# Performance work log

Measured on AMD Instinct MI355X. Metric: run time of the kernel, lower is better.

## Reference

```python
import jax, jax.numpy as jnp
import numpy as np

W_BITS = 8
A_BITS = 8


def sym_quant(x, num_bits):
    # Symmetric per-last-dim abs-max quantization (SymQuantizer.forward, ndim<=3,
    # layerwise=False): s = (2^(b-1)-1)/(max|x| + 1e-6); q = round(x*s)/(s+1e-6)
    max_abs = jnp.max(jnp.abs(x), axis=-1, keepdims=True)
    s = (2.0 ** (num_bits - 1) - 1.0) / (max_abs + 1e-6)
    return jnp.round(x * s) / (s + 1e-6)


def setup_inputs() -> dict:
    key = jax.random.key(0)
    kx, kw = jax.random.split(key)
    B, S, NX, NF = 4, 2048, 1600, 6400
    x = jax.random.normal(kx, (B, S, NX), dtype=jnp.float32)
    weight = 0.02 * jax.random.normal(kw, (NX, NF), dtype=jnp.float32)  # Conv1D: [nx, nf]
    bias = jnp.zeros((NF,), dtype=jnp.float32)
    return {"x": x, "weight": weight, "bias": bias}


def reference(x, weight, bias):
    # quantize weights per-row (over nf), quantize activations per-token (over nx)
    wq = sym_quant(weight, W_BITS)
    xq = sym_quant(x, A_BITS)
    # addmm(bias, x.view(-1, nx), weight) then reshape back
    return jnp.einsum("bsx,xf->bsf", xq, wq) + bias
```

## Files before the change

kernel.cpp:

```cpp
#include <hip/hip_runtime.h>
#include <stdint.h>

typedef _Float16 f16;
typedef _Float16 f16x4 __attribute__((ext_vector_type(4)));
typedef _Float16 f16x8 __attribute__((ext_vector_type(8)));
typedef float f32x4 __attribute__((ext_vector_type(4)));

#define K_DIM 1600
#define NF_DIM 6400
#define KPAD 1664
#define NKT 26
#define KPB (KPAD * 2)

#define BUFSZ 57344
#define BOFF 16384

__device__ __forceinline__ void async_copy16(const void* g, void* l) {
    __builtin_amdgcn_global_load_lds(
        (const __attribute__((address_space(1))) void*)(uintptr_t)g,
        (__attribute__((address_space(3))) void*)(uint32_t)(uintptr_t)l,
        16, 0, 0);
}

__device__ __forceinline__ float blockMax(float v, float* sm) {
#pragma unroll
    for (int off = 32; off > 0; off >>= 1)
        v = fmaxf(v, __shfl_down(v, off, 64));
    int wid = threadIdx.x >> 6, lane = threadIdx.x & 63;
    if (lane == 0) sm[wid] = v;
    __syncthreads();
    if (threadIdx.x == 0) {
        float m = sm[0];
        for (int i = 1; i < (int)(blockDim.x >> 6); ++i) m = fmaxf(m, sm[i]);
        sm[0] = m;
    }
    __syncthreads();
    return sm[0];
}

__global__ void quant_x_kernel(const float* __restrict__ x, f16* __restrict__ qx,
                               float* __restrict__ ax) {
    __shared__ float sm[4];
    size_t row = blockIdx.x;
    const float* xr = x + row * (size_t)K_DIM;
    float m = 0.f;
    const int n4 = K_DIM >> 2;
    for (int i = threadIdx.x; i < n4; i += blockDim.x) {
        float4 v = ((const float4*)xr)[i];
        m = fmaxf(fmaxf(fmaxf(fabsf(v.x), fabsf(v.y)), fmaxf(fabsf(v.z), fabsf(v.w))), m);
    }
    m = blockMax(m, sm);
    float s = 127.0f / (m + 1e-6f);
    if (threadIdx.x == 0) ax[row] = 1.0f / (s + 1e-6f);
    f16* qr = qx + row * (size_t)KPAD;
    for (int i = threadIdx.x; i < n4; i += blockDim.x) {
        float4 v = ((const float4*)xr)[i];
        f16x4 q;
        q[0] = (f16)rintf(v.x * s);
        q[1] = (f16)rintf(v.y * s);
        q[2] = (f16)rintf(v.z * s);
        q[3] = (f16)rintf(v.w * s);
        *(f16x4*)&qr[i * 4] = q;
    }
    if (threadIdx.x < 16) {
        f16x4 z = {};
        *(f16x4*)&qr[K_DIM + threadIdx.x * 4] = z;
    }
}

__global__ void wscale_kernel(const float* __restrict__ w, float* __restrict__ sw) {
    __shared__ float sm[4];
    size_t k = blockIdx.x;
    const float* wr = w + k * (size_t)NF_DIM;
    float m = 0.f;
    const int n4 = NF_DIM >> 2;
    for (int i = threadIdx.x; i < n4; i += blockDim.x) {
        float4 v = ((const float4*)wr)[i];
        m = fmaxf(fmaxf(fmaxf(fabsf(v.x), fabsf(v.y)), fmaxf(fabsf(v.z), fabsf(v.w))), m);
    }
    m = blockMax(m, sm);
    if (threadIdx.x == 0) sw[k] = 127.0f / (m + 1e-6f);
}

__global__ void wtq_kernel(const float* __restrict__ w, const float* __restrict__ sw,
                           f16* __restrict__ wqt) {
    __shared__ f16 t[64][80];
    int k0 = blockIdx.x * 64;
    int f0 = blockIdx.y * 64;
    int tid = threadIdx.x;
    if (k0 >= K_DIM) {
        int fr = tid >> 2;
        int ch = (tid & 3) << 4;
        float4 z = {};
        float4* dst = (float4*)&wqt[(size_t)(f0 + fr) * KPAD + k0 + ch];
        dst[0] = z;
        dst[1] = z;
        return;
    }
    int rr = tid >> 4;
    int cc = (tid & 15) << 2;
#pragma unroll
    for (int i = 0; i < 4; ++i) {
        int r = rr + i * 16;
        float s = sw[k0 + r];
        float inv = 1.0f / (s + 1e-6f);
        float4 v = *(const float4*)&w[(size_t)(k0 + r) * NF_DIM + f0 + cc];
        t[cc + 0][r] = (f16)(rintf(v.x * s) * inv);
        t[cc + 1][r] = (f16)(rintf(v.y * s) * inv);
        t[cc + 2][r] = (f16)(rintf(v.z * s) * inv);
        t[cc + 3][r] = (f16)(rintf(v.w * s) * inv);
    }
    __syncthreads();
    int fr = tid >> 2;
    int ch = (tid & 3) << 4;
    const float4* src = (const float4*)&t[fr][ch];
    float4* dst = (float4*)&wqt[(size_t)(f0 + fr) * KPAD + k0 + ch];
    dst[0] = src[0];
    dst[1] = src[1];
}

__global__ __launch_bounds__(512, 1) void gemm128x320(
    const f16* __restrict__ A,
    const f16* __restrict__ Bt,
    const float* __restrict__ ax,
    const float* __restrict__ bias,
    float* __restrict__ C, int M, int N) {
    extern __shared__ char lds[];

    const int tid = threadIdx.x;
    const int lane = tid & 63;
    const int wv = tid >> 6;
    const int wm = wv >> 2;
    const int wn = wv & 3;
    const int lr = lane & 15;
    const int lg = lane >> 4;

    const int bid = blockIdx.x;
    const int cpx = gridDim.x >> 3;
    const int swz = (bid & 7) * cpx + (bid >> 3);
    const int tm = swz & 63;
    const int tn = swz >> 6;
    const size_t m0 = (size_t)tm * 128, n0 = (size_t)tn * 320;

    const int srow8 = lane >> 3;
    const int sslot = (lane & 7) ^ srow8;
    const char* pA = (const char*)A + (m0 + (size_t)(wv * 8 + srow8)) * KPB + sslot * 16;
    const char* pB = (const char*)Bt + (n0 + (size_t)(wv * 8 + srow8)) * KPB + sslot * 16;
    const int L0 = wv * 1024 + lane * 16;

#define ST_A(bufo, t)                                                          \
    {                                                                          \
        const char* g_ = pA + (size_t)(t) * 128;                               \
        async_copy16(g_, lds + (bufo) + L0);                                   \
        async_copy16(g_ + (size_t)64 * KPB, lds + (bufo) + 8192 + L0);         \
    }
#define ST_B(bufo, t)                                                          \
    {                                                                          \
        const char* g_ = pB + (size_t)(t) * 128;                               \
        _Pragma("unroll") for (int c_ = 0; c_ < 5; ++c_)                       \
            async_copy16(g_ + (size_t)(c_ * 64) * KPB,                         \
                         lds + (bufo) + BOFF + c_ * 8192 + L0);                \
    }

    const int swz0 = ((lg) ^ (lr & 7)) << 4;
    const int swz1 = ((4 + lg) ^ (lr & 7)) << 4;
    const int rbA = (wm * 64 + lr) * 128;
    const int rbB = BOFF + wn * 10240 + lr * 128;

#define RD_A(dst, bufo, rowoff, sz)                                    \
    {                                                                  \
        const char* p_ = lds + (bufo) + rbA + (rowoff) + (sz);         \
        dst[0] = *(const f16x8*)(p_);                                  \
        dst[1] = *(const f16x8*)(p_ + 2048);                           \
    }
#define RD_B(dst, bufo, sz)                                            \
    {                                                                  \
        const char* p_ = lds + (bufo) + rbB + (sz);                    \
        _Pragma("unroll") for (int n_ = 0; n_ < 5; ++n_)               \
            dst[n_] = *(const f16x8*)(p_ + n_ * 2048);                 \
    }

#define BARRIER __builtin_amdgcn_s_barrier()
#define LGKM(n) asm volatile("s_waitcnt lgkmcnt(" #n ")" ::: "memory")
#define VM0 asm volatile("s_waitcnt vmcnt(0)" ::: "memory")
#define SB0 __builtin_amdgcn_sched_barrier(0)

#define MF25(AF, BF, R0)                                                          \
    {                                                                             \
        __builtin_amdgcn_s_setprio(1);                                            \
        _Pragma("unroll") for (int a_ = 0; a_ < 2; ++a_)                          \
        _Pragma("unroll") for (int n_ = 0; n_ < 5; ++n_)                          \
            acc[(R0) + a_][n_] = __builtin_amdgcn_mfma_f32_16x16x32_f16(          \
                AF[a_], BF[n_], acc[(R0) + a_][n_], 0, 0, 0);                     \
        __builtin_amdgcn_s_setprio(0);                                            \
    }

#define TILE(CUR, NXT, tcur, tnext)                                   \
    {                                                                 \
                     \
        RD_A(aN, CUR, 0, swz1);                                       \
        RD_B(B1, CUR, swz1);                                          \
        ST_A(NXT, tnext);                                             \
        LGKM(7); SB0;                               \
        MF25(aP, B0, 0);                                              \
                             \
        RD_A(aP, CUR, 4096, swz0);                                    \
        ST_B(NXT, tnext);                                             \
        LGKM(2); SB0;                               \
        MF25(aN, B1, 0);                                              \
                                           \
        RD_A(aN, CUR, 4096, swz1);                                    \
        LGKM(2); SB0;                         \
        MF25(aP, B0, 2);                                              \
            \
        VM0;                                                          \
        BARRIER; SB0;                           \
        RD_A(aP, NXT, 0, swz0);                                       \
        RD_B(B0, NXT, swz0);                                          \
        LGKM(7); SB0;                         \
        MF25(aN, B1, 2);                                              \
        BARRIER;                       \
    }

    f32x4 acc[4][5] = {};
    f16x8 aP[2], aN[2], B0[5], B1[5];

    ST_A(0, 0);
    ST_B(0, 0);
    VM0;
    BARRIER;
    RD_A(aP, 0, 0, swz0);
    RD_B(B0, 0, swz0);

    for (int i = 0; i < NKT / 2; ++i) {
        const int te = 2 * i + 1;
        const int to = (2 * i + 2 < NKT) ? 2 * i + 2 : NKT - 1;
        TILE(0, BUFSZ, 2 * i, te);
        TILE(BUFSZ, 0, 2 * i + 1, to);
    }
    asm volatile("s_waitcnt vmcnt(0) lgkmcnt(0)" ::: "memory");

    float bv[5];
#pragma unroll
    for (int n_ = 0; n_ < 5; ++n_) bv[n_] = bias[n0 + wn * 80 + n_ * 16 + lr];
#pragma unroll
    for (int a = 0; a < 4; ++a) {
#pragma unroll
        for (int j = 0; j < 4; ++j) {
            size_t row = m0 + wm * 64 + a * 16 + lg * 4 + j;
            float axv = ax[row];
            float* crow = C + row * (size_t)N + n0 + wn * 80;
#pragma unroll
            for (int n_ = 0; n_ < 5; ++n_)
                crow[n_ * 16 + lr] = acc[a][n_][j] * axv + bv[n_];
        }
    }
}

extern "C" void kernel_launch(void* const* d_in, const int* in_sizes, int n_in,
                              void* d_out, int out_size, void* d_ws, size_t ws_size,
                              hipStream_t stream) {
    const float* x = (const float*)d_in[0];
    const float* w = (const float*)d_in[1];
    const float* bias = (const float*)d_in[2];
    float* out = (float*)d_out;

    const int M = in_sizes[0] / K_DIM;
    const int N = NF_DIM;

    char* ws = (char*)d_ws;
    f16* qx = (f16*)ws;
    f16* wqt = (f16*)(ws + (size_t)M * KPAD * 2);
    float* ax = (float*)(ws + (size_t)M * KPAD * 2 + (size_t)N * KPAD * 2);
    float* sw = ax + M;

    quant_x_kernel<<<M, 256, 0, stream>>>(x, qx, ax);
    wscale_kernel<<<K_DIM, 256, 0, stream>>>(w, sw);
    wtq_kernel<<<dim3(KPAD / 64, NF_DIM / 64), 256, 0, stream>>>(w, sw, wqt);

    (void)hipFuncSetAttribute((const void*)gemm128x320,
                              hipFuncAttributeMaxDynamicSharedMemorySize, 2 * BUFSZ);
    gemm128x320<<<(M / 128) * (N / 320), 512, 2 * BUFSZ, stream>>>(qx, wqt, ax, bias, out, M, N);
}
```

Measured before the change: 254.9 us.

## Pre-swizzle quantized activations into MFMA fragment layout and load A directly to registers

The activation quantizer now processes 16 rows per block through LDS and writes the quantized values in a layout that already matches the per-lane MFMA A-fragment order. The GEMM then loads A fragments straight from global memory into registers, prefetching one K-tile ahead, and no longer stages A in LDS. Only B goes through a smaller double-buffered LDS. This removes the LDS traffic and bank pressure for A and restructures the wait and barrier schedule. In exchange it uses more VGPRs for the prefetched A fragments, relies on global-load latency being hidden, and the quantizer gains a large LDS footprint.

```diff
diff --git a/kernel.cpp b/kernel.cpp
--- a/kernel.cpp
+++ b/kernel.cpp
@@ -10,10 +10,10 @@
 #define NF_DIM 6400
 #define KPAD 1664
 #define NKT 26
+#define KB52 52
 #define KPB (KPAD * 2)
 
-#define BUFSZ 57344
-#define BOFF 16384
+#define BUFB 40960
 
 __device__ __forceinline__ void async_copy16(const void* g, void* l) {
     __builtin_amdgcn_global_load_lds(
@@ -38,33 +38,52 @@
     return sm[0];
 }
 
-__global__ void quant_x_kernel(const float* __restrict__ x, f16* __restrict__ qx,
+#define QSTRIDE 1604
+__global__ void quant_x_kernel(const float* __restrict__ x, f16* __restrict__ qxt,
                                float* __restrict__ ax) {
-    __shared__ float sm[4];
-    size_t row = blockIdx.x;
-    const float* xr = x + row * (size_t)K_DIM;
-    float m = 0.f;
-    const int n4 = K_DIM >> 2;
-    for (int i = threadIdx.x; i < n4; i += blockDim.x) {
-        float4 v = ((const float4*)xr)[i];
-        m = fmaxf(fmaxf(fmaxf(fabsf(v.x), fabsf(v.y)), fmaxf(fabsf(v.z), fabsf(v.w))), m);
-    }
-    m = blockMax(m, sm);
-    float s = 127.0f / (m + 1e-6f);
-    if (threadIdx.x == 0) ax[row] = 1.0f / (s + 1e-6f);
-    f16* qr = qx + row * (size_t)KPAD;
-    for (int i = threadIdx.x; i < n4; i += blockDim.x) {
-        float4 v = ((const float4*)xr)[i];
-        f16x4 q;
-        q[0] = (f16)rintf(v.x * s);
-        q[1] = (f16)rintf(v.y * s);
-        q[2] = (f16)rintf(v.z * s);
-        q[3] = (f16)rintf(v.w * s);
-        *(f16x4*)&qr[i * 4] = q;
-    }
-    if (threadIdx.x < 16) {
-        f16x4 z = {};
-        *(f16x4*)&qr[K_DIM + threadIdx.x * 4] = z;
+    extern __shared__ float xs[];
+    __shared__ float sm[16];
+    const int mb = blockIdx.x;
+    const int tid = threadIdx.x;
+    const float4* xb4 = (const float4*)(x + (size_t)mb * 16 * K_DIM);
+    float4* xs4 = (float4*)xs;
+#pragma unroll
+    for (int rr = 0; rr < 16; ++rr)
+        for (int i = tid; i < 400; i += 256)
+            xs4[rr * 401 + i] = xb4[rr * 400 + i];
+    __syncthreads();
+    {
+        int r = tid >> 4, si = tid & 15;
+        float m = 0.f;
+        const float4* row4 = (const float4*)(xs + r * QSTRIDE);
+        for (int j = si; j < 400; j += 16) {
+            float4 v = row4[j];
+            m = fmaxf(fmaxf(fmaxf(fabsf(v.x), fabsf(v.y)), fmaxf(fabsf(v.z), fabsf(v.w))), m);
+        }
+#pragma unroll
+        for (int o = 8; o > 0; o >>= 1) m = fmaxf(m, __shfl_xor(m, o, 64));
+        if (si == 0) sm[r] = m;
+    }
+    __syncthreads();
+    if (tid < 16) {
+        float s = 127.0f / (sm[tid] + 1e-6f);
+        ax[mb * 16 + tid] = 1.0f / (s + 1e-6f);
+        sm[tid] = s;
+    }
+    __syncthreads();
+    f16* outb = qxt + (size_t)mb * KB52 * 512;
+    for (int c = tid; c < KB52 * 64; c += 256) {
+        int kb = c >> 6, lane = c & 63;
+        int lr = lane & 15, lg = lane >> 4;
+        int k0 = kb * 32 + lg * 8;
+        f16x8 q = {};
+        if (k0 < K_DIM) {
+            float s = sm[lr];
+            const float* src = xs + lr * QSTRIDE + k0;
+#pragma unroll
+            for (int j = 0; j < 8; ++j) q[j] = (f16)rintf(src[j] * s);
+        }
+        *(f16x8*)(outb + (size_t)c * 8) = q;
     }
 }
 
@@ -119,8 +138,8 @@
     dst[1] = src[1];
 }
 
-__global__ __launch_bounds__(512, 1) void gemm128x320(
-    const f16* __restrict__ A,
+__global__ __launch_bounds__(512, 1) void gemm_ad(
+    const f16* __restrict__ Aq,
     const f16* __restrict__ Bt,
     const float* __restrict__ ax,
     const float* __restrict__ bias,
@@ -144,99 +163,88 @@
 
     const int srow8 = lane >> 3;
     const int sslot = (lane & 7) ^ srow8;
-    const char* pA = (const char*)A + (m0 + (size_t)(wv * 8 + srow8)) * KPB + sslot * 16;
     const char* pB = (const char*)Bt + (n0 + (size_t)(wv * 8 + srow8)) * KPB + sslot * 16;
     const int L0 = wv * 1024 + lane * 16;
-
-#define ST_A(bufo, t)                                                          \
-    {                                                                          \
-        const char* g_ = pA + (size_t)(t) * 128;                               \
-        async_copy16(g_, lds + (bufo) + L0);                                   \
-        async_copy16(g_ + (size_t)64 * KPB, lds + (bufo) + 8192 + L0);         \
-    }
 #define ST_B(bufo, t)                                                          \
     {                                                                          \
         const char* g_ = pB + (size_t)(t) * 128;                               \
         _Pragma("unroll") for (int c_ = 0; c_ < 5; ++c_)                       \
             async_copy16(g_ + (size_t)(c_ * 64) * KPB,                         \
-                         lds + (bufo) + BOFF + c_ * 8192 + L0);                \
-    }
-
-    const int swz0 = ((lg) ^ (lr & 7)) << 4;
-    const int swz1 = ((4 + lg) ^ (lr & 7)) << 4;
-    const int rbA = (wm * 64 + lr) * 128;
-    const int rbB = BOFF + wn * 10240 + lr * 128;
-
-#define RD_A(dst, bufo, rowoff, sz)                                    \
-    {                                                                  \
-        const char* p_ = lds + (bufo) + rbA + (rowoff) + (sz);         \
-        dst[0] = *(const f16x8*)(p_);                                  \
-        dst[1] = *(const f16x8*)(p_ + 2048);                           \
-    }
-#define RD_B(dst, bufo, sz)                                            \
-    {                                                                  \
-        const char* p_ = lds + (bufo) + rbB + (sz);                    \
-        _Pragma("unroll") for (int n_ = 0; n_ < 5; ++n_)               \
-            dst[n_] = *(const f16x8*)(p_ + n_ * 2048);                 \
+                         lds + (bufo) + c_ * 8192 + L0);                       \
+    }
+
+    const f16* aBase = Aq + (size_t)(tm * 8 + wm * 4) * (KB52 * 512) + lane * 8;
+#define LD_A(dst, t)                                                           \
+    {                                                                          \
+        _Pragma("unroll") for (int p_ = 0; p_ < 4; ++p_)                       \
+        _Pragma("unroll") for (int kk_ = 0; kk_ < 2; ++kk_)                    \
+            dst[p_][kk_] = *(const f16x8*)(aBase +                             \
+                (size_t)(p_ * KB52 + 2 * (t) + kk_) * 512);                    \
+    }
+
+    const int bdr0 = (wn * 80 + lr) * 128 + (((lg) ^ (lr & 7)) << 4);
+    const int bdr1 = (wn * 80 + lr) * 128 + (((4 + lg) ^ (lr & 7)) << 4);
+#define RD_B5(dst, bufo, off)                                                  \
+    {                                                                          \
+        const char* p_ = lds + (bufo) + (off);                                 \
+        _Pragma("unroll") for (int n_ = 0; n_ < 5; ++n_)                       \
+            dst[n_] = *(const f16x8*)(p_ + n_ * 2048);                         \
     }
 
 #define BARRIER __builtin_amdgcn_s_barrier()
 #define LGKM(n) asm volatile("s_waitcnt lgkmcnt(" #n ")" ::: "memory")
-#define VM0 asm volatile("s_waitcnt vmcnt(0)" ::: "memory")
+#define VM13 asm volatile("s_waitcnt vmcnt(13)" ::: "memory")
 #define SB0 __builtin_amdgcn_sched_barrier(0)
 
-#define MF25(AF, BF, R0)                                                          \
+#define MF10(A0_, A1_, BF, R0)                                                    \
     {                                                                             \
         __builtin_amdgcn_s_setprio(1);                                            \
-        _Pragma("unroll") for (int a_ = 0; a_ < 2; ++a_)                          \
-        _Pragma("unroll") for (int n_ = 0; n_ < 5; ++n_)                          \
-            acc[(R0) + a_][n_] = __builtin_amdgcn_mfma_f32_16x16x32_f16(          \
-                AF[a_], BF[n_], acc[(R0) + a_][n_], 0, 0, 0);                     \
+        _Pragma("unroll") for (int n_ = 0; n_ < 5; ++n_) {                        \
+            acc[(R0)][n_] = __builtin_amdgcn_mfma_f32_16x16x32_f16(               \
+                A0_, BF[n_], acc[(R0)][n_], 0, 0, 0);                             \
+            acc[(R0) + 1][n_] = __builtin_amdgcn_mfma_f32_16x16x32_f16(           \
+                A1_, BF[n_], acc[(R0) + 1][n_], 0, 0, 0);                         \
+        }                                                                         \
         __builtin_amdgcn_s_setprio(0);                                            \
     }
 
-#define TILE(CUR, NXT, tcur, tnext)                                   \
+#define TILE(CUR, NXT, AC, AN, t1, t2)                                \
     {                                                                 \
-                     \
-        RD_A(aN, CUR, 0, swz1);                                       \
-        RD_B(B1, CUR, swz1);                                          \
-        ST_A(NXT, tnext);                                             \
-        LGKM(7); SB0;                               \
-        MF25(aP, B0, 0);                                              \
-                             \
-        RD_A(aP, CUR, 4096, swz0);                                    \
-        ST_B(NXT, tnext);                                             \
-        LGKM(2); SB0;                               \
-        MF25(aN, B1, 0);                                              \
-                                           \
-        RD_A(aN, CUR, 4096, swz1);                                    \
-        LGKM(2); SB0;                         \
-        MF25(aP, B0, 2);                                              \
-            \
-        VM0;                                                          \
-        BARRIER; SB0;                           \
-        RD_A(aP, NXT, 0, swz0);                                       \
-        RD_B(B0, NXT, swz0);                                          \
-        LGKM(7); SB0;                         \
-        MF25(aN, B1, 2);                                              \
-        BARRIER;                       \
+                                        \
+        LD_A(AN, t1);                                                 \
+        RD_B5(B1, CUR, bdr1);                                         \
+        LGKM(5); SB0;                                                 \
+        MF10(AC[0][0], AC[1][0], B0, 0);                              \
+                      \
+        LGKM(0); SB0;                                                 \
+        BARRIER;                                                      \
+        ST_B(CUR, t2); SB0;                                           \
+        MF10(AC[2][0], AC[3][0], B0, 2);                              \
+                                                   \
+        MF10(AC[0][1], AC[1][1], B1, 0);                              \
+               \
+        VM13; SB0;                                                    \
+        BARRIER;                                                      \
+        RD_B5(B0, NXT, bdr0); SB0;                                    \
+        MF10(AC[2][1], AC[3][1], B1, 2);                              \
     }
 
     f32x4 acc[4][5] = {};
-    f16x8 aP[2], aN[2], B0[5], B1[5];
-
-    ST_A(0, 0);
+    f16x8 aC[4][2], aN[4][2], B0[5], B1[5];
+
     ST_B(0, 0);
-    VM0;
+    ST_B(BUFB, 1);
+    LD_A(aC, 0);
+    VM13;
     BARRIER;
-    RD_A(aP, 0, 0, swz0);
-    RD_B(B0, 0, swz0);
+    RD_B5(B0, 0, bdr0);
 
     for (int i = 0; i < NKT / 2; ++i) {
-        const int te = 2 * i + 1;
-        const int to = (2 * i + 2 < NKT) ? 2 * i + 2 : NKT - 1;
-        TILE(0, BUFSZ, 2 * i, te);
-        TILE(BUFSZ, 0, 2 * i + 1, to);
+        const int t1 = 2 * i + 1;
+        const int t2 = (2 * i + 2 < NKT) ? 2 * i + 2 : NKT - 1;
+        const int t3 = (2 * i + 3 < NKT) ? 2 * i + 3 : NKT - 1;
+        TILE(0, BUFB, aC, aN, t1, t2);
+        TILE(BUFB, 0, aN, aC, t2, t3);
     }
     asm volatile("s_waitcnt vmcnt(0) lgkmcnt(0)" ::: "memory");
 
@@ -269,16 +277,18 @@
     const int N = NF_DIM;
 
     char* ws = (char*)d_ws;
-    f16* qx = (f16*)ws;
-    f16* wqt = (f16*)(ws + (size_t)M * KPAD * 2);
-    float* ax = (float*)(ws + (size_t)M * KPAD * 2 + (size_t)N * KPAD * 2);
+    f16* qxt = (f16*)ws;
+    f16* wqt = (f16*)(ws + (size_t)(M / 16) * KB52 * 512 * 2);
+    float* ax = (float*)(ws + (size_t)(M / 16) * KB52 * 512 * 2 + (size_t)N * KPAD * 2);
     float* sw = ax + M;
 
-    quant_x_kernel<<<M, 256, 0, stream>>>(x, qx, ax);
+    (void)hipFuncSetAttribute((const void*)quant_x_kernel,
+                              hipFuncAttributeMaxDynamicSharedMemorySize, 16 * QSTRIDE * 4);
+    quant_x_kernel<<<M / 16, 256, 16 * QSTRIDE * 4, stream>>>(x, qxt, ax);
     wscale_kernel<<<K_DIM, 256, 0, stream>>>(w, sw);
     wtq_kernel<<<dim3(KPAD / 64, NF_DIM / 64), 256, 0, stream>>>(w, sw, wqt);
 
-    (void)hipFuncSetAttribute((const void*)gemm128x320,
-                              hipFuncAttributeMaxDynamicSharedMemorySize, 2 * BUFSZ);
-    gemm128x320<<<(M / 128) * (N / 320), 512, 2 * BUFSZ, stream>>>(qx, wqt, ax, bias, out, M, N);
-}
+    (void)hipFuncSetAttribute((const void*)gemm_ad,
+                              hipFuncAttributeMaxDynamicSharedMemorySize, 2 * BUFB);
+    gemm_ad<<<(M / 128) * (N / 320), 512, 2 * BUFB, stream>>>(qxt, wqt, ax, bias, out, M, N);
+}
```

Result: slower. 268.0 us (+5.2%).

## Restructure GEMM pipeline into four barrier-separated MFMA phases with split A/B buffers

Applied to the files above, without the earlier changes.

The LDS layout is split into separate double buffers for A and B, with B prefetched two tiles ahead and A one tile ahead. Each K tile now runs as four phases: read fragments, wait with lgkmcnt(0), barrier, run 10 MFMAs, barrier. This replaces the finer-grained lgkmcnt overlap schedule. The aim is a simpler, deeper prefetch for B, but the extra barriers and full LDS waits risk serializing LDS reads with MFMA issue.

```diff
diff --git a/kernel.cpp b/kernel.cpp
--- a/kernel.cpp
+++ b/kernel.cpp
@@ -12,8 +12,11 @@
 #define NKT 26
 #define KPB (KPAD * 2)
 
-#define BUFSZ 57344
-#define BOFF 16384
+#define BA0 0
+#define BA1 16384
+#define BB0 32768
+#define BB1 73728
+#define LDS_TOTAL 114688
 
 __device__ __forceinline__ void async_copy16(const void* g, void* l) {
     __builtin_amdgcn_global_load_lds(
@@ -159,13 +162,13 @@
         const char* g_ = pB + (size_t)(t) * 128;                               \
         _Pragma("unroll") for (int c_ = 0; c_ < 5; ++c_)                       \
             async_copy16(g_ + (size_t)(c_ * 64) * KPB,                         \
-                         lds + (bufo) + BOFF + c_ * 8192 + L0);                \
+                         lds + (bufo) + c_ * 8192 + L0);                       \
     }
 
     const int swz0 = ((lg) ^ (lr & 7)) << 4;
     const int swz1 = ((4 + lg) ^ (lr & 7)) << 4;
     const int rbA = (wm * 64 + lr) * 128;
-    const int rbB = BOFF + wn * 10240 + lr * 128;
+    const int rbB = (wn * 80 + lr) * 128;
 
 #define RD_A(dst, bufo, rowoff, sz)                                    \
     {                                                                  \
@@ -173,7 +176,7 @@
         dst[0] = *(const f16x8*)(p_);                                  \
         dst[1] = *(const f16x8*)(p_ + 2048);                           \
     }
-#define RD_B(dst, bufo, sz)                                            \
+#define RD_B5(dst, bufo, sz)                                           \
     {                                                                  \
         const char* p_ = lds + (bufo) + rbB + (sz);                    \
         _Pragma("unroll") for (int n_ = 0; n_ < 5; ++n_)               \
@@ -181,11 +184,11 @@
     }
 
 #define BARRIER __builtin_amdgcn_s_barrier()
-#define LGKM(n) asm volatile("s_waitcnt lgkmcnt(" #n ")" ::: "memory")
-#define VM0 asm volatile("s_waitcnt vmcnt(0)" ::: "memory")
+#define LGKM0 asm volatile("s_waitcnt lgkmcnt(0)" ::: "memory")
+#define VM5 asm volatile("s_waitcnt vmcnt(5)" ::: "memory")
 #define SB0 __builtin_amdgcn_sched_barrier(0)
 
-#define MF25(AF, BF, R0)                                                          \
+#define MF10(AF, BF, R0)                                                          \
     {                                                                             \
         __builtin_amdgcn_s_setprio(1);                                            \
         _Pragma("unroll") for (int a_ = 0; a_ < 2; ++a_)                          \
@@ -195,48 +198,50 @@
         __builtin_amdgcn_s_setprio(0);                                            \
     }
 
-#define TILE(CUR, NXT, tcur, tnext)                                   \
+#define TILE(bA, bAn, bB, tA, tB)                                     \
     {                                                                 \
-                     \
-        RD_A(aN, CUR, 0, swz1);                                       \
-        RD_B(B1, CUR, swz1);                                          \
-        ST_A(NXT, tnext);                                             \
-        LGKM(7); SB0;                               \
-        MF25(aP, B0, 0);                                              \
-                             \
-        RD_A(aP, CUR, 4096, swz0);                                    \
-        ST_B(NXT, tnext);                                             \
-        LGKM(2); SB0;                               \
-        MF25(aN, B1, 0);                                              \
-                                           \
-        RD_A(aN, CUR, 4096, swz1);                                    \
-        LGKM(2); SB0;                         \
-        MF25(aP, B0, 2);                                              \
-            \
-        VM0;                                                          \
-        BARRIER; SB0;                           \
-        RD_A(aP, NXT, 0, swz0);                                       \
-        RD_B(B0, NXT, swz0);                                          \
-        LGKM(7); SB0;                         \
-        MF25(aN, B1, 2);                                              \
-        BARRIER;                       \
+                                                             \
+        RD_A(aF, bA, 0, swz0);                                        \
+        RD_B5(Bf, bB, swz0);                                          \
+        ST_A(bAn, tA);                                                \
+        BARRIER; LGKM0; SB0;                                          \
+        MF10(aF, Bf, 0);                                              \
+        BARRIER;                                                      \
+                                                             \
+        RD_A(aG, bA, 4096, swz0);                                     \
+        BARRIER; LGKM0; SB0;                                          \
+        MF10(aG, Bf, 2);                                              \
+        BARRIER;                                                      \
+                                                             \
+        RD_A(aF, bA, 0, swz1);                                        \
+        RD_B5(Bg, bB, swz1);                                          \
+        BARRIER; LGKM0; SB0;                                          \
+        MF10(aF, Bg, 0);                                              \
+        BARRIER;                                                      \
+                                                             \
+        RD_A(aG, bA, 4096, swz1);                                     \
+        ST_B(bB, tB);                                                 \
+        VM5;                                                          \
+        BARRIER; LGKM0; SB0;                                          \
+        MF10(aG, Bg, 2);                                              \
+        BARRIER;                                                      \
     }
 
     f32x4 acc[4][5] = {};
-    f16x8 aP[2], aN[2], B0[5], B1[5];
-
-    ST_A(0, 0);
-    ST_B(0, 0);
-    VM0;
+    f16x8 aF[2], aG[2], Bf[5], Bg[5];
+
+    ST_A(BA0, 0);
+    ST_B(BB0, 0);
+    ST_B(BB1, 1);
+    VM5;
     BARRIER;
-    RD_A(aP, 0, 0, swz0);
-    RD_B(B0, 0, swz0);
 
     for (int i = 0; i < NKT / 2; ++i) {
         const int te = 2 * i + 1;
-        const int to = (2 * i + 2 < NKT) ? 2 * i + 2 : NKT - 1;
-        TILE(0, BUFSZ, 2 * i, te);
-        TILE(BUFSZ, 0, 2 * i + 1, to);
+        const int tb2 = (2 * i + 2 < NKT) ? 2 * i + 2 : NKT - 1;
+        const int tb3 = (2 * i + 3 < NKT) ? 2 * i + 3 : NKT - 1;
+        TILE(BA0, BA1, BB0, te, tb2);
+        TILE(BA1, BA0, BB1, tb2, tb3);
     }
     asm volatile("s_waitcnt vmcnt(0) lgkmcnt(0)" ::: "memory");
 
@@ -279,6 +284,6 @@
     wtq_kernel<<<dim3(KPAD / 64, NF_DIM / 64), 256, 0, stream>>>(w, sw, wqt);
 
     (void)hipFuncSetAttribute((const void*)gemm128x320,
-                              hipFuncAttributeMaxDynamicSharedMemorySize, 2 * BUFSZ);
-    gemm128x320<<<(M / 128) * (N / 320), 512, 2 * BUFSZ, stream>>>(qx, wqt, ax, bias, out, M, N);
-}
+                              hipFuncAttributeMaxDynamicSharedMemorySize, LDS_TOTAL);
+    gemm128x320<<<(M / 128) * (N / 320), 512, LDS_TOTAL, stream>>>(qx, wqt, ax, bias, out, M, N);
+}
```

New measurement: 233.3 us, median of 2. 1.09x faster.
